# Kernel optimization log

Hardware: AMD Instinct MI355X
Metric: run time of the kernel (lower is better)

The kernel has to match this reference:

```python
import jax, jax.numpy as jnp
import numpy as np
from functools import partial

N, F_IN, P, OUT, E = 100000, 8, 12, 32, 3200000


def setup_inputs() -> dict:
    key = jax.random.key(0)
    ks = jax.random.split(key, 20)
    x = jax.random.normal(ks[0], (N, F_IN, P), dtype=jnp.float32)
    edge_index = jax.random.randint(ks[1], (2, E), 0, N, dtype=jnp.int64)
    edge_weight = jax.random.uniform(ks[2], (E,), dtype=jnp.float32)
    s = 1.0 / np.sqrt(F_IN)
    s2 = 1.0 / np.sqrt(2 * OUT)
    u = lambda k, sh, sc: jax.random.uniform(k, sh, jnp.float32, -sc, sc)
    params = dict(
        Wz=u(ks[3], (F_IN, OUT), s), bz=u(ks[4], (OUT,), s),
        Wr=u(ks[5], (F_IN, OUT), s), br=u(ks[6], (OUT,), s),
        Wh=u(ks[7], (F_IN, OUT), s), bh=u(ks[8], (OUT,), s),
        Lz=u(ks[9], (2 * OUT, OUT), s2), lbz=u(ks[10], (OUT,), s2),
        Lr=u(ks[11], (2 * OUT, OUT), s2), lbr=u(ks[12], (OUT,), s2),
        Lh=u(ks[13], (2 * OUT, OUT), s2), lbh=u(ks[14], (OUT,), s2),
        att=jax.random.uniform(ks[15], (P,), jnp.float32),
        Wp=u(ks[16], (OUT, 1), 1.0 / np.sqrt(OUT)), bp=u(ks[17], (1,), 1.0 / np.sqrt(OUT)),
    )
    return {"x": x, "edge_index": edge_index, "edge_weight": edge_weight, **params}


def reference(x, edge_index, edge_weight, Wz, bz, Wr, br, Wh, bh,
              Lz, lbz, Lr, lbr, Lh, lbh, att, Wp, bp):
    n = x.shape[0]
    # GCN normalization with self-loops: D^-1/2 (A + I) D^-1/2
    loop = jnp.arange(n)
    src = jnp.concatenate([edge_index[0], loop])
    dst = jnp.concatenate([edge_index[1], loop])
    w = jnp.concatenate([edge_weight, jnp.ones((n,), edge_weight.dtype)])
    deg = jax.ops.segment_sum(w, dst, num_segments=n)
    dinv = jnp.where(deg > 0, jax.lax.rsqrt(jnp.maximum(deg, 1e-30)), 0.0)
    norm = dinv[src] * w * dinv[dst]  # [E+N]

    def prop(X):  # gather-scale-scatter aggregation, X: [N, OUT]
        return jax.ops.segment_sum(X[src] * norm[:, None], dst, num_segments=n)

    def cell(H, Xt):  # TGCN GRU cell, Xt: [N, F_IN]
        cz = prop(Xt @ Wz) + bz
        cr = prop(Xt @ Wr) + br
        ch = prop(Xt @ Wh) + bh
        Z = jax.nn.sigmoid(jnp.concatenate([cz, H], axis=1) @ Lz + lbz)
        R = jax.nn.sigmoid(jnp.concatenate([cr, H], axis=1) @ Lr + lbr)
        Ht = jnp.tanh(jnp.concatenate([ch, R * H], axis=1) @ Lh + lbh)
        return Z * H + (1.0 - Z) * Ht

    probs = jax.nn.softmax(att)
    Xts = jnp.moveaxis(x, -1, 0)  # [P, N, F_IN]

    def scan_fn(carry, inp):
        H, acc = carry
        Xt, p = inp
        Hn = cell(H, Xt)
        return (Hn, acc + p * Hn), None

    H0 = jnp.zeros((n, OUT), x.dtype)
    (_, Hacc), _ = jax.lax.scan(scan_fn, (H0, H0), (Xts, probs))

    h = jax.nn.relu(Hacc)  # dropout is identity in eval mode
    delta = h @ Wp + bp  # [N, 1]
    out = jax.nn.relu(delta + x[:, 1, -1:])
    return out
```

## Files before the change

kernel.cpp:

```cpp
#include <hip/hip_runtime.h>
#include <cstddef>

typedef __attribute__((ext_vector_type(8))) short bf16x8;
typedef __attribute__((ext_vector_type(4))) float f32x4;

#define MFMA_B16(a, b, c) __builtin_amdgcn_mfma_f32_16x16x32_bf16(a, b, c, 0, 0, 0)

#define DEV_INLINE __device__ __forceinline__

#define NPB 128
#define NPB_SHIFT 7
#define NOCT 8
#define OCT_SHIFT 14

#define QSCALE (127.0f / 6.0f)
#define QDEC   (6.0f / 127.0f)

DEV_INLINE float sigf(float x) { return 1.0f / (1.0f + __expf(-x)); }
DEV_INLINE float tanh_fast(float x) { float e2 = __expf(2.0f * x); return 1.0f - 2.0f / (e2 + 1.0f); }

DEV_INLINE unsigned short f2bf(float f) {
    union { float f; unsigned u; } v; v.f = f;
    unsigned r = v.u + 0x7fffu + ((v.u >> 16) & 1u);
    return (unsigned short)(r >> 16);
}

__global__ __launch_bounds__(256) void k_cast(const float* __restrict__ x,
                                              signed char* __restrict__ Xb8, int n) {
    __shared__ float s[64 * 97];
    const int tid = threadIdx.x;
    const int nbase = blockIdx.x * 64;
    const int lim = n * 96;
    const int base_elem = nbase * 96;

#pragma unroll
    for (int j = 0; j < 6; j++) {
        int g = j * 1024 + tid * 4;
        int gg = base_elem + g;
        if (gg + 4 <= lim) {
            float4 v = *(const float4*)(x + gg);
            int node = g / 96;
            int e = g - node * 96;
            float* p = &s[node * 97 + e];
            p[0] = v.x; p[1] = v.y; p[2] = v.z; p[3] = v.w;
        }
    }
    __syncthreads();

    const int nloc = tid >> 2;
    const int c = tid & 3;
    const int node = nbase + nloc;
    if (node < n) {
        const float* row = &s[nloc * 97];
        signed char* orow = Xb8 + (size_t)node * 96;
#pragma unroll
        for (int q = 0; q < 3; q++) {
            int t = c + 4 * q;
            unsigned w0 = 0u, w1 = 0u;
#pragma unroll
            for (int f = 0; f < 4; f++) {
                int qv = __float2int_rn(row[f * 12 + t] * QSCALE);
                qv = max(-127, min(127, qv));
                w0 |= ((unsigned)qv & 0xFFu) << (8 * f);
            }
#pragma unroll
            for (int f = 4; f < 8; f++) {
                int qv = __float2int_rn(row[f * 12 + t] * QSCALE);
                qv = max(-127, min(127, qv));
                w1 |= ((unsigned)qv & 0xFFu) << (8 * (f - 4));
            }
            uint2 vv = {w0, w1};
            *(uint2*)(orow + c * 8 + 32 * q) = vv;
        }
    }
}

__global__ __launch_bounds__(1024) void k_p3(const int* __restrict__ ei,
                                             const float* __restrict__ ew,
                                             unsigned* __restrict__ bucketCursor,
                                             uint2* __restrict__ EB, int E) {
    __shared__ unsigned hist[1024];
    __shared__ unsigned bbase[1024];
    const int t = threadIdx.x;
    hist[t] = 0u;
    __syncthreads();
    const int base = blockIdx.x * 8192 + t * 8;
    unsigned key[8]; float w[8]; unsigned rk[8]; int bkt[8];
#pragma unroll
    for (int q = 0; q < 8; q++) {
        int e = base + q;
        if (e < E) {
            int d = ei[(size_t)E + e];
            int s = ei[e];
            w[q] = ew[e];
            bkt[q] = d >> NPB_SHIFT;
            key[q] = (unsigned)s | ((unsigned)(d & (NPB - 1)) << 20);
            rk[q] = atomicAdd(&hist[bkt[q]], 1u);
        } else bkt[q] = -1;
    }
    __syncthreads();
    if (hist[t]) bbase[t] = atomicAdd(bucketCursor + t, hist[t]);
    __syncthreads();
#pragma unroll
    for (int q = 0; q < 8; q++) {
        if (bkt[q] >= 0) {
            uint2 it; it.x = key[q]; it.y = __float_as_uint(w[q]);
            EB[(size_t)bbase[bkt[q]] + rk[q]] = it;
        }
    }
}

__global__ __launch_bounds__(1024) void k_p2(const unsigned* __restrict__ bucketCursor,
                                             unsigned* __restrict__ bucketCnt,
                                             unsigned* __restrict__ bucketBase,
                                             int* __restrict__ rowptr,
                                             int NB, int N, int E, int CAP) {
    __shared__ unsigned ts[1024];
    const int t = threadIdx.x;
    unsigned v = (t < NB) ? (bucketCursor[t] - (unsigned)(t * CAP)) : 0u;
    ts[t] = v;
    __syncthreads();
    for (int off = 1; off < 1024; off <<= 1) {
        unsigned a = ts[t];
        unsigned b = (t >= off) ? ts[t - off] : 0u;
        __syncthreads();
        ts[t] = a + b;
        __syncthreads();
    }
    if (t < NB) {
        bucketBase[t] = ts[t] - v;
        bucketCnt[t] = v;
    }
    if (t == 0) rowptr[N] = E;
}

__global__ __launch_bounds__(1024) void k_p4(const uint2* __restrict__ EB,
                                             const unsigned* __restrict__ bucketBase,
                                             const unsigned* __restrict__ bucketCnt,
                                             int* __restrict__ rowptr,
                                             float* __restrict__ dinv,
                                             uint2* __restrict__ cedge, int N, int CAP) {
    __shared__ unsigned cnt[NPB * NOCT];
    __shared__ unsigned lrow[NPB * NOCT];
    __shared__ float degs[NPB];
    __shared__ float sdinv[NPB];
    const int t = threadIdx.x;
    const int b = blockIdx.x;
    const size_t sbase = (size_t)b * CAP;
    const unsigned bbase = bucketBase[b];
    const unsigned bcnt = bucketCnt[b];
    cnt[t] = 0u;
    if (t < NPB) degs[t] = 0.0f;
    __syncthreads();

    unsigned key[8]; float w[8]; unsigned rk[8];
#pragma unroll
    for (int q = 0; q < 8; q++) {
        unsigned i = (unsigned)t + (unsigned)q * 1024u;
        if (i < bcnt) {
            uint2 it = EB[sbase + i];
            key[q] = it.x;
            w[q] = __uint_as_float(it.y);
            unsigned dl = it.x >> 20;
            unsigned oct = (it.x & 0xFFFFFu) >> OCT_SHIFT;
            rk[q] = atomicAdd(&cnt[dl * NOCT + oct], 1u);
            atomicAdd(&degs[dl], w[q]);
        }
    }
    __syncthreads();

    unsigned own = cnt[t];
    lrow[t] = own;
    __syncthreads();
    for (int off = 1; off < NPB * NOCT; off <<= 1) {
        unsigned a = lrow[t];
        unsigned c = (t >= off) ? lrow[t - off] : 0u;
        __syncthreads();
        lrow[t] = a + c;
        __syncthreads();
    }
    lrow[t] = lrow[t] - own;
    __syncthreads();
    if (t < NPB) {
        float dv = rsqrtf(degs[t] + 1.0f);
        sdinv[t] = dv;
        int node = b * NPB + t;
        if (node < N) { rowptr[node] = (int)(bbase + lrow[t * NOCT]); dinv[node] = dv; }
    }
    __syncthreads();

#pragma unroll
    for (int q = 0; q < 8; q++) {
        unsigned i = (unsigned)t + (unsigned)q * 1024u;
        if (i < bcnt) {
            unsigned dl = key[q] >> 20;
            unsigned src = key[q] & 0xFFFFFu;
            unsigned oct = src >> OCT_SHIFT;
            unsigned pos = bbase + lrow[dl * NOCT + oct] + rk[q];
            uint2 it; it.x = src; it.y = __float_as_uint(w[q] * sdinv[dl]);
            cedge[pos] = it;
        }
    }
}

__global__ __launch_bounds__(256) void k_pull(const signed char* __restrict__ Xb8,
                                              const float* __restrict__ dinv,
                                              const int* __restrict__ rowptr,
                                              const uint2* __restrict__ cedge,
                                              unsigned short* __restrict__ Xp, int n) {
    int gid = blockIdx.x * 256 + threadIdx.x;
    int d = gid >> 2;
    int c = gid & 3;
    if (d >= n) return;
    float di = dinv[d];
    float sl = di * di * QDEC;
    float a[24];
    {
        const signed char* xr = Xb8 + (size_t)d * 96 + c * 8;
#pragma unroll
        for (int q = 0; q < 3; q++) {
            uint2 v = *(const uint2*)(xr + 32 * q);
            a[q * 8 + 0] = sl * (float)(signed char)(v.x);
            a[q * 8 + 1] = sl * (float)(signed char)(v.x >> 8);
            a[q * 8 + 2] = sl * (float)(signed char)(v.x >> 16);
            a[q * 8 + 3] = sl * (float)(signed char)(v.x >> 24);
            a[q * 8 + 4] = sl * (float)(signed char)(v.y);
            a[q * 8 + 5] = sl * (float)(signed char)(v.y >> 8);
            a[q * 8 + 6] = sl * (float)(signed char)(v.y >> 16);
            a[q * 8 + 7] = sl * (float)(signed char)(v.y >> 24);
        }
    }
    int lo = rowptr[d], hi = rowptr[d + 1];
    int e = lo;

#define ACC8(vv, cf, q)                                                     \
    do {                                                                    \
        a[(q) * 8 + 0] += (cf) * (float)(signed char)((vv).x);              \
        a[(q) * 8 + 1] += (cf) * (float)(signed char)((vv).x >> 8);         \
        a[(q) * 8 + 2] += (cf) * (float)(signed char)((vv).x >> 16);        \
        a[(q) * 8 + 3] += (cf) * (float)(signed char)((vv).x >> 24);        \
        a[(q) * 8 + 4] += (cf) * (float)(signed char)((vv).y);              \
        a[(q) * 8 + 5] += (cf) * (float)(signed char)((vv).y >> 8);         \
        a[(q) * 8 + 6] += (cf) * (float)(signed char)((vv).y >> 16);        \
        a[(q) * 8 + 7] += (cf) * (float)(signed char)((vv).y >> 24);        \
    } while (0)

    for (; e + 4 <= hi; e += 4) {
        uint2 se0 = cedge[e + 0];
        uint2 se1 = cedge[e + 1];
        uint2 se2 = cedge[e + 2];
        uint2 se3 = cedge[e + 3];
        float ds0 = dinv[se0.x];
        float ds1 = dinv[se1.x];
        float ds2 = dinv[se2.x];
        float ds3 = dinv[se3.x];
        const signed char* x0 = Xb8 + (size_t)se0.x * 96 + c * 8;
        const signed char* x1 = Xb8 + (size_t)se1.x * 96 + c * 8;
        const signed char* x2 = Xb8 + (size_t)se2.x * 96 + c * 8;
        const signed char* x3 = Xb8 + (size_t)se3.x * 96 + c * 8;
        uint2 v0[3], v1[3], v2[3], v3[3];
#pragma unroll
        for (int q = 0; q < 3; q++) v0[q] = *(const uint2*)(x0 + 32 * q);
#pragma unroll
        for (int q = 0; q < 3; q++) v1[q] = *(const uint2*)(x1 + 32 * q);
#pragma unroll
        for (int q = 0; q < 3; q++) v2[q] = *(const uint2*)(x2 + 32 * q);
#pragma unroll
        for (int q = 0; q < 3; q++) v3[q] = *(const uint2*)(x3 + 32 * q);
        float c0 = __uint_as_float(se0.y) * ds0 * QDEC;
        float c1 = __uint_as_float(se1.y) * ds1 * QDEC;
        float c2 = __uint_as_float(se2.y) * ds2 * QDEC;
        float c3 = __uint_as_float(se3.y) * ds3 * QDEC;
#pragma unroll
        for (int q = 0; q < 3; q++) ACC8(v0[q], c0, q);
#pragma unroll
        for (int q = 0; q < 3; q++) ACC8(v1[q], c1, q);
#pragma unroll
        for (int q = 0; q < 3; q++) ACC8(v2[q], c2, q);
#pragma unroll
        for (int q = 0; q < 3; q++) ACC8(v3[q], c3, q);
    }
    for (; e < hi; e++) {
        uint2 se = cedge[e];
        float cf = __uint_as_float(se.y) * dinv[se.x] * QDEC;
        const signed char* xs = Xb8 + (size_t)se.x * 96 + c * 8;
        uint2 vv[3];
#pragma unroll
        for (int q = 0; q < 3; q++) vv[q] = *(const uint2*)(xs + 32 * q);
#pragma unroll
        for (int q = 0; q < 3; q++) ACC8(vv[q], cf, q);
    }
#undef ACC8

    unsigned short* o = Xp + (size_t)d * 96 + c * 8;
#pragma unroll
    for (int q = 0; q < 3; q++) {
        unsigned w0 = (unsigned)f2bf(a[q * 8 + 0]) | ((unsigned)f2bf(a[q * 8 + 1]) << 16);
        unsigned w1 = (unsigned)f2bf(a[q * 8 + 2]) | ((unsigned)f2bf(a[q * 8 + 3]) << 16);
        unsigned w2 = (unsigned)f2bf(a[q * 8 + 4]) | ((unsigned)f2bf(a[q * 8 + 5]) << 16);
        unsigned w3 = (unsigned)f2bf(a[q * 8 + 6]) | ((unsigned)f2bf(a[q * 8 + 7]) << 16);
        uint4 vv = {w0, w1, w2, w3};
        *(uint4*)(o + 32 * q) = vv;
    }
}

__global__ __launch_bounds__(256) void k_wprep(const float* __restrict__ Wz, const float* __restrict__ Wr,
                                               const float* __restrict__ Wh,
                                               const float* __restrict__ Lz, const float* __restrict__ Lr,
                                               const float* __restrict__ Lh,
                                               const float* __restrict__ bz, const float* __restrict__ br,
                                               const float* __restrict__ bh,
                                               const float* __restrict__ lbz, const float* __restrict__ lbr,
                                               const float* __restrict__ lbh,
                                               float* __restrict__ WC,
                                               unsigned* __restrict__ bucketCursor, int NB, int CAP) {
    int tid = threadIdx.x;
    for (int b = tid; b < NB; b += 256) bucketCursor[b] = (unsigned)(b * CAP);
    for (int e = tid; e < 2048; e += 256) {
        int j = e >> 5, k = e & 31;
        const float* L = (j < 32) ? Lz : Lr;
        WC[e] = L[(32 + k) * 32 + (j & 31)];
    }
    for (int e = tid; e < 512; e += 256) {
        int j = e >> 3, f = e & 7;
        const float* L = (j < 32) ? Lz : Lr;
        const float* W = (j < 32) ? Wz : Wr;
        int jj = j & 31;
        float s = 0.0f;
        for (int i = 0; i < 32; i++) s += W[f * 32 + i] * L[i * 32 + jj];
        WC[2048 + e] = s;
    }
    for (int e = tid; e < 1024; e += 256) {
        int j = e >> 5, k = e & 31;
        WC[2560 + e] = Lh[(32 + k) * 32 + j];
    }
    for (int e = tid; e < 256; e += 256) {
        int j = e >> 3, f = e & 7;
        float s = 0.0f;
        for (int i = 0; i < 32; i++) s += Wh[f * 32 + i] * Lh[i * 32 + j];
        WC[3584 + e] = s;
    }
    if (tid < 64) {
        int j = tid;
        const float* L = (j < 32) ? Lz : Lr;
        const float* b = (j < 32) ? bz : br;
        const float* lb = (j < 32) ? lbz : lbr;
        int jj = j & 31;
        float s = lb[jj];
        for (int i = 0; i < 32; i++) s += b[i] * L[i * 32 + jj];
        WC[3840 + j] = s;
    }
    if (tid < 32) {
        float s = lbh[tid];
        for (int i = 0; i < 32; i++) s += bh[i] * Lh[i * 32 + tid];
        WC[3904 + tid] = s;
    }
}

__global__ __launch_bounds__(64) void k_gru(const unsigned short* __restrict__ Xp,
                                            const float* __restrict__ x,
                                            const float* __restrict__ WC,
                                            const float* __restrict__ att,
                                            const float* __restrict__ Wp,
                                            const float* __restrict__ bp,
                                            float* __restrict__ out, int n) {
    __shared__ __align__(16) unsigned short sH[16 * 40];
    __shared__ __align__(16) unsigned short sRH[16 * 40];
    __shared__ __align__(16) unsigned short sXp[12 * 16 * 8];
    __shared__ __align__(16) unsigned short zblk[8];

    const int l = threadIdx.x;
    const int lo16 = l & 15;
    const int g = l >> 4;
    const int base = blockIdx.x * 16;

#pragma unroll
    for (int j = 0; j < 3; j++) {
        int i = l + 64 * j;
        int nd = min(base + (i & 15), n - 1);
        int q = i >> 4;
        uint4 v = *(const uint4*)(Xp + (size_t)nd * 96 + q * 8);
        *(uint4*)(&sXp[q * 128 + (i & 15) * 8]) = v;
    }
    for (int i = l; i < 16 * 40 / 2; i += 64) ((unsigned*)sH)[i] = 0u;
    if (l < 4) ((unsigned*)zblk)[l] = 0u;
    __syncthreads();

    const float* WZRH_H = WC;
    const float* WZR_X = WC + 2048;
    const float* WH_H = WC + 2560;
    const float* WH_X = WC + 3584;
    const float* BZR = WC + 3840;
    const float* BH = WC + 3904;

    bf16x8 wZRH[4], wZRX[4], wHH[2], wHX[2];
#pragma unroll
    for (int mt = 0; mt < 4; mt++) {
        int j = mt * 16 + lo16;
#pragma unroll
        for (int e = 0; e < 8; e++) {
            wZRH[mt][e] = (short)f2bf(WZRH_H[j * 32 + g * 8 + e]);
            wZRX[mt][e] = (g == 0) ? (short)f2bf(WZR_X[j * 8 + e]) : (short)0;
        }
    }
#pragma unroll
    for (int mt = 0; mt < 2; mt++) {
        int j = mt * 16 + lo16;
#pragma unroll
        for (int e = 0; e < 8; e++) {
            wHH[mt][e] = (short)f2bf(WH_H[j * 32 + g * 8 + e]);
            wHX[mt][e] = (g == 0) ? (short)f2bf(WH_X[j * 8 + e]) : (short)0;
        }
    }

    float bzr[4][4], bhh[2][4], wpr[2][4];
#pragma unroll
    for (int mt = 0; mt < 4; mt++)
#pragma unroll
        for (int r = 0; r < 4; r++) bzr[mt][r] = BZR[mt * 16 + 4 * g + r];
#pragma unroll
    for (int mt = 0; mt < 2; mt++)
#pragma unroll
        for (int r = 0; r < 4; r++) {
            bhh[mt][r] = BH[mt * 16 + 4 * g + r];
            wpr[mt][r] = Wp[mt * 16 + 4 * g + r];
        }

    float am = att[0];
    for (int t = 1; t < 12; t++) am = fmaxf(am, att[t]);
    float ad = 0.0f;
    for (int t = 0; t < 12; t++) ad += __expf(att[t] - am);
    float inv_ad = 1.0f / ad;

    float H[2][4], acc[2][4];
#pragma unroll
    for (int mt = 0; mt < 2; mt++)
#pragma unroll
        for (int r = 0; r < 4; r++) { H[mt][r] = 0.0f; acc[mt][r] = 0.0f; }

    const f32x4 kc = {0.0f, 0.0f, 0.0f, 0.0f};

#pragma unroll 1
    for (int t = 0; t < 12; t++) {
        float pt = __expf(att[t] - am) * inv_ad;

        bf16x8 bH = *(const bf16x8*)(&sH[lo16 * 40 + g * 8]);
        const unsigned short* px = (g == 0) ? &sXp[t * 128 + lo16 * 8] : &zblk[0];
        bf16x8 bX = *(const bf16x8*)px;

        float Z[2][4];
#pragma unroll
        for (int mt = 0; mt < 2; mt++) {
            f32x4 d = MFMA_B16(wZRH[mt], bH, kc);
            d = MFMA_B16(wZRX[mt], bX, d);
#pragma unroll
            for (int r = 0; r < 4; r++) Z[mt][r] = sigf(d[r] + bzr[mt][r]);
        }

#pragma unroll
        for (int mt = 2; mt < 4; mt++) {
            f32x4 d = MFMA_B16(wZRH[mt], bH, kc);
            d = MFMA_B16(wZRX[mt], bX, d);
            float rh[4];
#pragma unroll
            for (int r = 0; r < 4; r++)
                rh[r] = H[mt - 2][r] * sigf(d[r] + bzr[mt][r]);
            uint2 w;
            w.x = (unsigned)f2bf(rh[0]) | ((unsigned)f2bf(rh[1]) << 16);
            w.y = (unsigned)f2bf(rh[2]) | ((unsigned)f2bf(rh[3]) << 16);
            *(uint2*)(&sRH[lo16 * 40 + (mt - 2) * 16 + 4 * g]) = w;
        }

        bf16x8 bR = *(const bf16x8*)(&sRH[lo16 * 40 + g * 8]);

#pragma unroll
        for (int mt = 0; mt < 2; mt++) {
            f32x4 d = MFMA_B16(wHH[mt], bR, kc);
            d = MFMA_B16(wHX[mt], bX, d);
#pragma unroll
            for (int r = 0; r < 4; r++) {
                float T = tanh_fast(d[r] + bhh[mt][r]);
                float z = Z[mt][r];
                float h = T + z * (H[mt][r] - T);
                H[mt][r] = h;
                acc[mt][r] += pt * h;
            }
            uint2 w;
            w.x = (unsigned)f2bf(H[mt][0]) | ((unsigned)f2bf(H[mt][1]) << 16);
            w.y = (unsigned)f2bf(H[mt][2]) | ((unsigned)f2bf(H[mt][3]) << 16);
            *(uint2*)(&sH[lo16 * 40 + mt * 16 + 4 * g]) = w;
        }
    }

    float p = 0.0f;
#pragma unroll
    for (int mt = 0; mt < 2; mt++)
#pragma unroll
        for (int r = 0; r < 4; r++) p += fmaxf(acc[mt][r], 0.0f) * wpr[mt][r];
    p += __shfl_xor(p, 16);
    p += __shfl_xor(p, 32);
    if (l < 16) {
        int nd = base + l;
        if (nd < n) out[nd] = fmaxf(p + bp[0] + x[(size_t)nd * 96 + 23], 0.0f);
    }
}

static inline size_t align_up(size_t v, size_t a) { return (v + a - 1) & ~(a - 1); }

extern "C" void kernel_launch(void* const* d_in, const int* in_sizes, int n_in,
                              void* d_out, int out_size, void* d_ws, size_t ws_size,
                              hipStream_t stream) {
    const float* x   = (const float*)d_in[0];
    const int*   ei  = (const int*)d_in[1];
    const float* ew  = (const float*)d_in[2];
    const float* Wz  = (const float*)d_in[3];
    const float* bz  = (const float*)d_in[4];
    const float* Wr  = (const float*)d_in[5];
    const float* br  = (const float*)d_in[6];
    const float* Wh  = (const float*)d_in[7];
    const float* bh  = (const float*)d_in[8];
    const float* Lz  = (const float*)d_in[9];
    const float* lbz = (const float*)d_in[10];
    const float* Lr  = (const float*)d_in[11];
    const float* lbr = (const float*)d_in[12];
    const float* Lh  = (const float*)d_in[13];
    const float* lbh = (const float*)d_in[14];
    const float* att = (const float*)d_in[15];
    const float* Wp  = (const float*)d_in[16];
    const float* bp  = (const float*)d_in[17];
    float* out = (float*)d_out;

    const int N = in_sizes[0] / 96;
    const int E = in_sizes[2];
    const int NB = (N + NPB - 1) / NPB;

    char* ws = (char*)d_ws;
    size_t off = 0;
    float* dinv   = (float*)(ws + off); off = align_up(off + (size_t)N * 4, 256);
    int*   rowptr = (int*)  (ws + off); off = align_up(off + (size_t)(N + 1) * 4, 256);
    unsigned* bucketCnt    = (unsigned*)(ws + off); off = align_up(off + 1024 * 4, 256);
    unsigned* bucketBase   = (unsigned*)(ws + off); off = align_up(off + 1024 * 4, 256);
    unsigned* bucketCursor = (unsigned*)(ws + off); off = align_up(off + 1024 * 4, 256);
    uint2* cedge  = (uint2*)(ws + off); off = align_up(off + (size_t)E * 8, 256);
    signed char* Xb8 = (signed char*)(ws + off);
    size_t xb8_off = off;              off = align_up(off + (size_t)N * 96, 256);
    unsigned short* Xp = (unsigned short*)(ws + off); off = align_up(off + (size_t)N * 96 * 2, 256);
    float* WC     = (float*)(ws + off); off = align_up(off + 3936 * 4, 256);

    size_t overlay_bytes = (off - xb8_off);
    int CAP = (int)(overlay_bytes / ((size_t)NB * 8));
    CAP &= ~7;
    uint2* EB = (uint2*)Xb8;

    int eb8 = (E + 8191) / 8192;

    k_wprep<<<1, 256, 0, stream>>>(Wz, Wr, Wh, Lz, Lr, Lh, bz, br, bh, lbz, lbr, lbh,
                                   WC, bucketCursor, NB, CAP);
    k_p3<<<eb8, 1024, 0, stream>>>(ei, ew, bucketCursor, EB, E);
    k_p2<<<1, 1024, 0, stream>>>(bucketCursor, bucketCnt, bucketBase, rowptr, NB, N, E, CAP);
    k_p4<<<NB, 1024, 0, stream>>>(EB, bucketBase, bucketCnt, rowptr, dinv, cedge, N, CAP);
    k_cast<<<(N + 63) / 64, 256, 0, stream>>>(x, Xb8, N);
    k_pull<<<(N * 4 + 255) / 256, 256, 0, stream>>>(Xb8, dinv, rowptr, cedge, Xp, N);
    k_gru<<<(N + 15) / 16, 64, 0, stream>>>(Xp, x, WC, att, Wp, bp, out, N);
}
```

Before: 294.3 us.

## Use hardware bf16 pack, fast reciprocal, and 4-wave GRU blocks

Replaces the software round-to-nearest bf16 packing with the v_cvt_pk_bf16_f32 instruction in the pull and GRU kernels. Sigmoid and tanh now use the hardware approximate reciprocal instead of a full division. The GRU kernel runs four independent 16-node waves per 256-thread block, each with its own shared-memory slices, instead of one 64-thread block per 16 nodes, which cuts block count and scheduling overhead. The approximate reciprocal adds a little error to the gate activations.

```diff
diff --git a/kernel.cpp b/kernel.cpp
--- a/kernel.cpp
+++ b/kernel.cpp
@@ -16,13 +16,20 @@
 #define QSCALE (127.0f / 6.0f)
 #define QDEC   (6.0f / 127.0f)
 
-DEV_INLINE float sigf(float x) { return 1.0f / (1.0f + __expf(-x)); }
-DEV_INLINE float tanh_fast(float x) { float e2 = __expf(2.0f * x); return 1.0f - 2.0f / (e2 + 1.0f); }
+DEV_INLINE float rcp_fast(float x) { return __builtin_amdgcn_rcpf(x); }
+DEV_INLINE float sigf(float x) { return rcp_fast(1.0f + __expf(-x)); }
+DEV_INLINE float tanh_fast(float x) { return 1.0f - 2.0f * rcp_fast(__expf(2.0f * x) + 1.0f); }
 
 DEV_INLINE unsigned short f2bf(float f) {
     union { float f; unsigned u; } v; v.f = f;
     unsigned r = v.u + 0x7fffu + ((v.u >> 16) & 1u);
     return (unsigned short)(r >> 16);
+}
+
+DEV_INLINE unsigned cvt_pk_bf16(float lo, float hi) {
+    unsigned r;
+    asm("v_cvt_pk_bf16_f32 %0, %1, %2" : "=v"(r) : "v"(lo), "v"(hi));
+    return r;
 }
 
 __global__ __launch_bounds__(256) void k_cast(const float* __restrict__ x,
@@ -295,10 +302,10 @@
     unsigned short* o = Xp + (size_t)d * 96 + c * 8;
 #pragma unroll
     for (int q = 0; q < 3; q++) {
-        unsigned w0 = (unsigned)f2bf(a[q * 8 + 0]) | ((unsigned)f2bf(a[q * 8 + 1]) << 16);
-        unsigned w1 = (unsigned)f2bf(a[q * 8 + 2]) | ((unsigned)f2bf(a[q * 8 + 3]) << 16);
-        unsigned w2 = (unsigned)f2bf(a[q * 8 + 4]) | ((unsigned)f2bf(a[q * 8 + 5]) << 16);
-        unsigned w3 = (unsigned)f2bf(a[q * 8 + 6]) | ((unsigned)f2bf(a[q * 8 + 7]) << 16);
+        unsigned w0 = cvt_pk_bf16(a[q * 8 + 0], a[q * 8 + 1]);
+        unsigned w1 = cvt_pk_bf16(a[q * 8 + 2], a[q * 8 + 3]);
+        unsigned w2 = cvt_pk_bf16(a[q * 8 + 4], a[q * 8 + 5]);
+        unsigned w3 = cvt_pk_bf16(a[q * 8 + 6], a[q * 8 + 7]);
         uint4 vv = {w0, w1, w2, w3};
         *(uint4*)(o + 32 * q) = vv;
     }
@@ -357,22 +364,28 @@
     }
 }
 
-__global__ __launch_bounds__(64) void k_gru(const unsigned short* __restrict__ Xp,
-                                            const float* __restrict__ x,
-                                            const float* __restrict__ WC,
-                                            const float* __restrict__ att,
-                                            const float* __restrict__ Wp,
-                                            const float* __restrict__ bp,
-                                            float* __restrict__ out, int n) {
-    __shared__ __align__(16) unsigned short sH[16 * 40];
-    __shared__ __align__(16) unsigned short sRH[16 * 40];
-    __shared__ __align__(16) unsigned short sXp[12 * 16 * 8];
-    __shared__ __align__(16) unsigned short zblk[8];
-
-    const int l = threadIdx.x;
+__global__ __launch_bounds__(256) void k_gru(const unsigned short* __restrict__ Xp,
+                                             const float* __restrict__ x,
+                                             const float* __restrict__ WC,
+                                             const float* __restrict__ att,
+                                             const float* __restrict__ Wp,
+                                             const float* __restrict__ bp,
+                                             float* __restrict__ out, int n) {
+    __shared__ __align__(16) unsigned short sH[4][16 * 40];
+    __shared__ __align__(16) unsigned short sRH[4][16 * 40];
+    __shared__ __align__(16) unsigned short sXp[4][12 * 16 * 8];
+    __shared__ __align__(16) unsigned short zblk[4][8];
+
+    const int tid = threadIdx.x;
+    const int wv = tid >> 6;
+    const int l = tid & 63;
     const int lo16 = l & 15;
     const int g = l >> 4;
-    const int base = blockIdx.x * 16;
+    const int base = blockIdx.x * 64 + wv * 16;
+
+    unsigned short* SH = sH[wv];
+    unsigned short* SRH = sRH[wv];
+    unsigned short* SXP = sXp[wv];
 
 #pragma unroll
     for (int j = 0; j < 3; j++) {
@@ -380,10 +393,10 @@
         int nd = min(base + (i & 15), n - 1);
         int q = i >> 4;
         uint4 v = *(const uint4*)(Xp + (size_t)nd * 96 + q * 8);
-        *(uint4*)(&sXp[q * 128 + (i & 15) * 8]) = v;
-    }
-    for (int i = l; i < 16 * 40 / 2; i += 64) ((unsigned*)sH)[i] = 0u;
-    if (l < 4) ((unsigned*)zblk)[l] = 0u;
+        *(uint4*)(&SXP[q * 128 + (i & 15) * 8]) = v;
+    }
+    for (int i = l; i < 16 * 40 / 2; i += 64) ((unsigned*)SH)[i] = 0u;
+    if (l < 4) ((unsigned*)zblk[wv])[l] = 0u;
     __syncthreads();
 
     const float* WZRH_H = WC;
@@ -430,7 +443,7 @@
     for (int t = 1; t < 12; t++) am = fmaxf(am, att[t]);
     float ad = 0.0f;
     for (int t = 0; t < 12; t++) ad += __expf(att[t] - am);
-    float inv_ad = 1.0f / ad;
+    float inv_ad = rcp_fast(ad);
 
     float H[2][4], acc[2][4];
 #pragma unroll
@@ -444,8 +457,8 @@
     for (int t = 0; t < 12; t++) {
         float pt = __expf(att[t] - am) * inv_ad;
 
-        bf16x8 bH = *(const bf16x8*)(&sH[lo16 * 40 + g * 8]);
-        const unsigned short* px = (g == 0) ? &sXp[t * 128 + lo16 * 8] : &zblk[0];
+        bf16x8 bH = *(const bf16x8*)(&SH[lo16 * 40 + g * 8]);
+        const unsigned short* px = (g == 0) ? &SXP[t * 128 + lo16 * 8] : &zblk[wv][0];
         bf16x8 bX = *(const bf16x8*)px;
 
         float Z[2][4];
@@ -466,12 +479,12 @@
             for (int r = 0; r < 4; r++)
                 rh[r] = H[mt - 2][r] * sigf(d[r] + bzr[mt][r]);
             uint2 w;
-            w.x = (unsigned)f2bf(rh[0]) | ((unsigned)f2bf(rh[1]) << 16);
-            w.y = (unsigned)f2bf(rh[2]) | ((unsigned)f2bf(rh[3]) << 16);
-            *(uint2*)(&sRH[lo16 * 40 + (mt - 2) * 16 + 4 * g]) = w;
-        }
-
-        bf16x8 bR = *(const bf16x8*)(&sRH[lo16 * 40 + g * 8]);
+            w.x = cvt_pk_bf16(rh[0], rh[1]);
+            w.y = cvt_pk_bf16(rh[2], rh[3]);
+            *(uint2*)(&SRH[lo16 * 40 + (mt - 2) * 16 + 4 * g]) = w;
+        }
+
+        bf16x8 bR = *(const bf16x8*)(&SRH[lo16 * 40 + g * 8]);
 
 #pragma unroll
         for (int mt = 0; mt < 2; mt++) {
@@ -486,9 +499,9 @@
                 acc[mt][r] += pt * h;
             }
             uint2 w;
-            w.x = (unsigned)f2bf(H[mt][0]) | ((unsigned)f2bf(H[mt][1]) << 16);
-            w.y = (unsigned)f2bf(H[mt][2]) | ((unsigned)f2bf(H[mt][3]) << 16);
-            *(uint2*)(&sH[lo16 * 40 + mt * 16 + 4 * g]) = w;
+            w.x = cvt_pk_bf16(H[mt][0], H[mt][1]);
+            w.y = cvt_pk_bf16(H[mt][2], H[mt][3]);
+            *(uint2*)(&SH[lo16 * 40 + mt * 16 + 4 * g]) = w;
         }
     }
 
@@ -561,5 +574,5 @@
     k_p4<<<NB, 1024, 0, stream>>>(EB, bucketBase, bucketCnt, rowptr, dinv, cedge, N, CAP);
     k_cast<<<(N + 63) / 64, 256, 0, stream>>>(x, Xb8, N);
     k_pull<<<(N * 4 + 255) / 256, 256, 0, stream>>>(Xb8, dinv, rowptr, cedge, Xp, N);
-    k_gru<<<(N + 15) / 16, 64, 0, stream>>>(Xp, x, WC, att, Wp, bp, out, N);
-}
+    k_gru<<<(N + 63) / 64, 256, 0, stream>>>(Xp, x, WC, att, Wp, bp, out, N);
+}
```

Measured after the change: 261.3 us, median of 3. 11.2% less time.
